# Optimization experiments

Hardware: AMD Instinct MI355X
Metric: run time of the kernel (lower is better)

The kernel has to match this reference:

```python
import jax, jax.numpy as jnp
import numpy as np
from jax import lax

PATCH = 3
RBF_SIGMA = 0.06 * PATCH ** 2      # module scales sigma by patch_size**2
SIG2 = RBF_SIGMA ** 2


def _unfold(img):
    # torch.nn.Unfold(kernel_size=3, stride=1): (b, c*9, N) with N=(H-2)*(W-2).
    # Channel ordering inside d differs from torch but distances sum over d,
    # so any consistent patch flattening yields identical math.
    p = lax.conv_general_dilated_patches(img, (PATCH, PATCH), (1, 1), 'VALID')
    b, d = p.shape[0], p.shape[1]
    return p.reshape(b, d, -1)  # (b, d, N)


def _kernel_mean(xu, yu):
    # mean over (N, M) of exp(-||x_i - y_j||^2 / sigma^2), via the
    # ||x||^2 + ||y||^2 - 2<x,y> expansion (avoids the (b,d,N,M) diff tensor).
    sqx = jnp.sum(xu * xu, axis=1)                   # (b, N)
    sqy = jnp.sum(yu * yu, axis=1)                   # (b, M)
    gram = jnp.einsum('bdn,bdm->bnm', xu, yu)        # (b, N, M)
    d2 = sqx[:, :, None] + sqy[:, None, :] - 2.0 * gram
    return jnp.mean(jnp.exp(-d2 / SIG2), axis=(1, 2))  # (b,)


def setup_inputs() -> dict:
    key = jax.random.key(0)
    kx, ky = jax.random.split(key)
    x = jax.random.normal(kx, (8, 3, 64, 64), dtype=jnp.float32)
    y = jax.random.normal(ky, (8, 3, 64, 64), dtype=jnp.float32)
    return {"x": x, "y": y}


def reference(x, y):
    xu = _unfold(x)
    yu = _unfold(y)
    batch_loss = (-2.0 * _kernel_mean(xu, yu)
                  + _kernel_mean(xu, xu)
                  + _kernel_mean(yu, yu))       # (b,)
    return jnp.mean(batch_loss)                 # batch_reduction='mean'
```

## Files before the change

### kernel.cpp

```cpp
#include <hip/hip_runtime.h>
#include <hip/hip_bf16.h>


#define NP    3844
#define NPAD  3968
#define KP    32

#define W_XY  7688
#define W_ALL 15624
#define NBLK  15624

static constexpr float L_F   = 4.9475824173972215f;
static constexpr float C2L_F = 9.895164834794443f;

using bf16x8 = __attribute__((ext_vector_type(8))) short;
using f32x4  = __attribute__((ext_vector_type(4))) float;

#define MFMA16(a, b, c) __builtin_amdgcn_mfma_f32_16x16x32_bf16((a), (b), (c), 0, 0, 0)

__device__ inline unsigned short f2bf(float f) {
    union { float f; unsigned u; } v; v.f = f;
    unsigned r = v.u + 0x7FFFu + ((v.u >> 16) & 1u);
    return (unsigned short)(r >> 16);
}
__device__ inline float bf2f(unsigned short h) {
    union { unsigned u; float f; } v; v.u = ((unsigned)h) << 16;
    return v.f;
}
__device__ inline void pack_store(unsigned short* dst, const unsigned short* v) {
    uint4* d = (uint4*)dst;
#pragma unroll
    for (int q = 0; q < 4; ++q) {
        unsigned w0 = (unsigned)v[8 * q + 0] | ((unsigned)v[8 * q + 1] << 16);
        unsigned w1 = (unsigned)v[8 * q + 2] | ((unsigned)v[8 * q + 3] << 16);
        unsigned w2 = (unsigned)v[8 * q + 4] | ((unsigned)v[8 * q + 5] << 16);
        unsigned w3 = (unsigned)v[8 * q + 6] | ((unsigned)v[8 * q + 7] << 16);
        d[q] = make_uint4(w0, w1, w2, w3);
    }
}

__global__ __launch_bounds__(256) void gp_prep(const float* __restrict__ x,
                                               const float* __restrict__ y,
                                               unsigned short* __restrict__ Am,
                                               unsigned short* __restrict__ Bm) {
    int i = blockIdx.x * 256 + threadIdx.x;
    if (i >= 16 * NPAD) return;
    int n = i % NPAD, im = i / NPAD;
    int b = im & 7;
    const float* src = (im >> 3) ? y : x;

    const unsigned short ONE = f2bf(1.0f);
    unsigned short hA[32], hB[32];
#pragma unroll
    for (int k = 0; k < 32; ++k) { hA[k] = 0; hB[k] = 0; }

    if (n < NP) {
        int r = n / 62, c = n % 62;
        float s = 0.0f;
#pragma unroll
        for (int ch = 0; ch < 3; ++ch)
#pragma unroll
            for (int pr = 0; pr < 3; ++pr)
#pragma unroll
                for (int pc = 0; pc < 3; ++pc) {
                    int k = ch * 9 + pr * 3 + pc;
                    float v = src[(((b * 3 + ch) * 64) + r + pr) * 64 + (c + pc)];
                    unsigned short ah = f2bf(C2L_F * v);
                    unsigned short bh = f2bf(v);
                    hA[k] = ah; hB[k] = bh;
                    s = fmaf(bf2f(ah), bf2f(bh), s);
                }
        float p = -0.5f * s;
        hA[27] = f2bf(p); hA[28] = f2bf(p - bf2f(hA[27]));
        hA[29] = ONE; hA[30] = ONE;
        hB[27] = ONE; hB[28] = ONE;
        hB[29] = f2bf(p); hB[30] = f2bf(p - bf2f(hB[29]));
    } else {
        hA[27] = f2bf(-1e30f); hA[29] = ONE; hA[30] = ONE;
        hB[27] = ONE; hB[28] = ONE; hB[29] = f2bf(-1e30f);
    }

    pack_store(Am + (size_t)i * KP, hA);
    pack_store(Bm + (size_t)i * KP, hB);
}

template<int OFF>
__device__ inline bf16x8 gload(const unsigned short* p) {
    bf16x8 r;
    asm volatile("global_load_dwordx4 %0, %1, off offset:%2"
                 : "=v"(r) : "v"(p), "i"(OFF));
    return r;
}

#define BODY(BHC)                                                            \
    do {                                                                     \
        const f32x4 Z = {0.f, 0.f, 0.f, 0.f};                                \
        f32x4 g0 = MFMA16(ah0, BHC, Z); f32x4 g1 = MFMA16(ah1, BHC, Z);      \
        f32x4 g2 = MFMA16(ah2, BHC, Z); f32x4 g3 = MFMA16(ah3, BHC, Z);      \
        f32x4 g4 = MFMA16(ah4, BHC, Z); f32x4 g5 = MFMA16(ah5, BHC, Z);      \
        f32x4 g6 = MFMA16(ah6, BHC, Z); f32x4 g7 = MFMA16(ah7, BHC, Z);      \
        float m0 = fmaxf(fmaxf(fmaxf(g0[0], g0[1]), g0[2]), g0[3]);          \
        float m1 = fmaxf(fmaxf(fmaxf(g1[0], g1[1]), g1[2]), g1[3]);          \
        float m2 = fmaxf(fmaxf(fmaxf(g2[0], g2[1]), g2[2]), g2[3]);          \
        float m3 = fmaxf(fmaxf(fmaxf(g3[0], g3[1]), g3[2]), g3[3]);          \
        float m4 = fmaxf(fmaxf(fmaxf(g4[0], g4[1]), g4[2]), g4[3]);          \
        float m5 = fmaxf(fmaxf(fmaxf(g5[0], g5[1]), g5[2]), g5[3]);          \
        float m6 = fmaxf(fmaxf(fmaxf(g6[0], g6[1]), g6[2]), g6[3]);          \
        float m7 = fmaxf(fmaxf(fmaxf(g7[0], g7[1]), g7[2]), g7[3]);          \
        float mm = fmaxf(fmaxf(fmaxf(fmaxf(fmaxf(fmaxf(fmaxf(m0, m1), m2),   \
                         m3), m4), m5), m6), m7);                            \
        if (__any(mm > -40.0f)) {                                            \
            s0 += __builtin_amdgcn_exp2f(g0[0]); s1 += __builtin_amdgcn_exp2f(g0[1]); \
            s2 += __builtin_amdgcn_exp2f(g0[2]); s3 += __builtin_amdgcn_exp2f(g0[3]); \
            s0 += __builtin_amdgcn_exp2f(g1[0]); s1 += __builtin_amdgcn_exp2f(g1[1]); \
            s2 += __builtin_amdgcn_exp2f(g1[2]); s3 += __builtin_amdgcn_exp2f(g1[3]); \
            s0 += __builtin_amdgcn_exp2f(g2[0]); s1 += __builtin_amdgcn_exp2f(g2[1]); \
            s2 += __builtin_amdgcn_exp2f(g2[2]); s3 += __builtin_amdgcn_exp2f(g2[3]); \
            s0 += __builtin_amdgcn_exp2f(g3[0]); s1 += __builtin_amdgcn_exp2f(g3[1]); \
            s2 += __builtin_amdgcn_exp2f(g3[2]); s3 += __builtin_amdgcn_exp2f(g3[3]); \
            s0 += __builtin_amdgcn_exp2f(g4[0]); s1 += __builtin_amdgcn_exp2f(g4[1]); \
            s2 += __builtin_amdgcn_exp2f(g4[2]); s3 += __builtin_amdgcn_exp2f(g4[3]); \
            s0 += __builtin_amdgcn_exp2f(g5[0]); s1 += __builtin_amdgcn_exp2f(g5[1]); \
            s2 += __builtin_amdgcn_exp2f(g5[2]); s3 += __builtin_amdgcn_exp2f(g5[3]); \
            s0 += __builtin_amdgcn_exp2f(g6[0]); s1 += __builtin_amdgcn_exp2f(g6[1]); \
            s2 += __builtin_amdgcn_exp2f(g6[2]); s3 += __builtin_amdgcn_exp2f(g6[3]); \
            s0 += __builtin_amdgcn_exp2f(g7[0]); s1 += __builtin_amdgcn_exp2f(g7[1]); \
            s2 += __builtin_amdgcn_exp2f(g7[2]); s3 += __builtin_amdgcn_exp2f(g7[3]); \
        }                                                                    \
    } while (0)

#define STEPN(N, CURREG)                                                     \
    do {                                                                     \
        asm volatile("s_waitcnt vmcnt(" #N ")" : "+v"(CURREG));              \
        __builtin_amdgcn_sched_barrier(0);                                   \
        BODY(CURREG);                                                        \
    } while (0)

__global__ __launch_bounds__(64, 4) void gp_pairs18(const unsigned short* __restrict__ Am,
                                                    const unsigned short* __restrict__ Bm,
                                                    float* __restrict__ part) {
    const int phys = blockIdx.x;
    const int w = (phys & 7) * 1953 + (phys >> 3);

    const int l = threadIdx.x & 63;
    const int l15 = l & 15, lhi = l >> 4;

    int type, b, bx, by, slot;
    float wt = 1.0f;
    if (w < W_XY) {
        type = 0; b = w / 961;
        int rr = w % 961; by = rr / 31; bx = rr % 31;
        slot = rr;
    } else {
        int v = w - W_XY;
        type = 1 + v / 3968;
        int r = v % 3968; b = r / 496; int t2 = r % 496;
        by = (int)((sqrtf(8.0f * (float)t2 + 1.0f) - 1.0f) * 0.5f);
        while ((by + 1) * (by + 2) / 2 <= t2) ++by;
        while (by * (by + 1) / 2 > t2) --by;
        bx = t2 - by * (by + 1) / 2;
        wt = (bx == by) ? 1.0f : 2.0f;
        slot = t2;
    }
    int imA, imB;
    if (type == 0)      { imA = b;     imB = 8 + b; }
    else if (type == 1) { imA = b;     imB = b;     }
    else                { imA = 8 + b; imB = 8 + b; }

    const size_t eA = ((size_t)(imA * NPAD + bx * 128 + l15)) * KP + lhi * 8;
    const size_t eB = ((size_t)(imB * NPAD + by * 128 + l15)) * KP + lhi * 8;
    const unsigned short* pA0 = Am + eA;
    const unsigned short* pA4 = pA0 + 2048;
    const unsigned short* pB0 = Bm + eB;
    const unsigned short* pB4 = pB0 + 2048;

    bf16x8 ah0 = gload<0>(pA0),    ah1 = gload<1024>(pA0);
    bf16x8 ah2 = gload<2048>(pA0), ah3 = gload<3072>(pA0);
    bf16x8 ah4 = gload<0>(pA4),    ah5 = gload<1024>(pA4);
    bf16x8 ah6 = gload<2048>(pA4), ah7 = gload<3072>(pA4);

    bf16x8 b0 = gload<0>(pB0),    b1 = gload<1024>(pB0);
    bf16x8 b2 = gload<2048>(pB0), b3 = gload<3072>(pB0);
    bf16x8 b4 = gload<0>(pB4),    b5 = gload<1024>(pB4);
    bf16x8 b6 = gload<2048>(pB4), b7 = gload<3072>(pB4);

    asm volatile("s_waitcnt vmcnt(8)"
                 : "+v"(ah0), "+v"(ah1), "+v"(ah2), "+v"(ah3),
                   "+v"(ah4), "+v"(ah5), "+v"(ah6), "+v"(ah7));
    __builtin_amdgcn_sched_barrier(0);

    float s0 = 0.f, s1 = 0.f, s2 = 0.f, s3 = 0.f;

    STEPN(7, b0);
    STEPN(6, b1);
    STEPN(5, b2);
    STEPN(4, b3);
    STEPN(3, b4);
    STEPN(2, b5);
    STEPN(1, b6);
    STEPN(0, b7);

    float sacc = wt * ((s0 + s1) + (s2 + s3));

#pragma unroll
    for (int o = 32; o > 0; o >>= 1) sacc += __shfl_down(sacc, o, 64);
    if (l == 0) part[(type * 8 + b) * 1024 + slot] = sacc;
}

__global__ __launch_bounds__(256) void gp_reduce(const float* __restrict__ part,
                                                 float* __restrict__ acc) {
    const int bkt = blockIdx.x;
    const int cnt = (bkt < 8) ? 961 : 496;
    const float* p = part + bkt * 1024;
    float s = 0.0f;
    for (int i = threadIdx.x; i < cnt; i += 256) s += p[i];
#pragma unroll
    for (int o = 32; o > 0; o >>= 1) s += __shfl_down(s, o, 64);
    __shared__ float red[4];
    if ((threadIdx.x & 63) == 0) red[threadIdx.x >> 6] = s;
    __syncthreads();
    if (threadIdx.x == 0) acc[bkt] = (red[0] + red[1]) + (red[2] + red[3]);
}

__global__ void gp_final(const float* __restrict__ acc, float* __restrict__ out) {
    if (threadIdx.x == 0) {
        double s = 0.0;
        for (int b = 0; b < 8; ++b)
            s += -2.0 * (double)acc[b] + (double)acc[8 + b] + (double)acc[16 + b];
        out[0] = (float)(s / (8.0 * (double)NP * (double)NP));
    }
}

extern "C" void kernel_launch(void* const* d_in, const int* in_sizes, int n_in,
                              void* d_out, int out_size, void* d_ws, size_t ws_size,
                              hipStream_t stream) {
    const float* x = (const float*)d_in[0];
    const float* y = (const float*)d_in[1];
    const size_t MSZ = (size_t)16 * NPAD * KP;
    unsigned short* Am = (unsigned short*)d_ws;
    unsigned short* Bm = Am + MSZ;
    float* acc = (float*)(Bm + MSZ);
    float* part = acc + 32;

    gp_prep<<<(16 * NPAD) / 256, 256, 0, stream>>>(x, y, Am, Bm);
    gp_pairs18<<<NBLK, 64, 0, stream>>>(Am, Bm, part);
    gp_reduce<<<24, 256, 0, stream>>>(part, acc);
    gp_final<<<1, 1, 0, stream>>>(acc, (float*)d_out);
}
```

Before: 39.56 us.

## Fuse reduction into pair kernel via last-block atomic and pack four waves per block

The pair kernel now runs four 64-lane waves per 256-thread block (3906 blocks instead of 15624 single-wave blocks), with an adjusted XCD-aware block-to-work mapping. The separate reduce and final kernels are removed. Each block writes its partials, bumps an atomic counter that gp_prep resets, and the last block to finish performs the 24-bucket reduction and writes the output. This removes two kernel launches and their gaps, at the cost of a block-level barrier in every block and a serialized tail reduction in one block.

```diff
diff --git a/kernel.cpp b/kernel.cpp
--- a/kernel.cpp
+++ b/kernel.cpp
@@ -8,7 +8,7 @@
 
 #define W_XY  7688
 #define W_ALL 15624
-#define NBLK  15624
+#define NBLK  3906
 
 static constexpr float L_F   = 4.9475824173972215f;
 static constexpr float C2L_F = 9.895164834794443f;
@@ -42,7 +42,9 @@
 __global__ __launch_bounds__(256) void gp_prep(const float* __restrict__ x,
                                                const float* __restrict__ y,
                                                unsigned short* __restrict__ Am,
-                                               unsigned short* __restrict__ Bm) {
+                                               unsigned short* __restrict__ Bm,
+                                               unsigned int* __restrict__ ctl) {
+    if (blockIdx.x == 0 && threadIdx.x == 0) ctl[0] = 0u;
     int i = blockIdx.x * 256 + threadIdx.x;
     if (i >= 16 * NPAD) return;
     int n = i % NPAD, im = i / NPAD;
@@ -136,14 +138,24 @@
         BODY(CURREG);                                                        \
     } while (0)
 
-__global__ __launch_bounds__(64, 4) void gp_pairs18(const unsigned short* __restrict__ Am,
-                                                    const unsigned short* __restrict__ Bm,
-                                                    float* __restrict__ part) {
+__global__ __launch_bounds__(256, 4) void gp_pairs19(const unsigned short* __restrict__ Am,
+                                                     const unsigned short* __restrict__ Bm,
+                                                     float* __restrict__ part,
+                                                     unsigned int* __restrict__ ctl,
+                                                     float* __restrict__ out) {
+    __shared__ int   sIdx[4];
+    __shared__ float sVal[4];
+    __shared__ int   sLast;
+    __shared__ float bsum[24];
+
     const int phys = blockIdx.x;
-    const int w = (phys & 7) * 1953 + (phys >> 3);
-
-    const int l = threadIdx.x & 63;
+    const int xcd = phys & 7, oi = phys >> 3;
+    const int blk = (xcd < 2 ? xcd * 489 : 2 * 489 + (xcd - 2) * 488) + oi;
+
+    const int t = threadIdx.x;
+    const int wv = t >> 6, l = t & 63;
     const int l15 = l & 15, lhi = l >> 4;
+    const int w = blk * 4 + wv;
 
     int type, b, bx, by, slot;
     float wt = 1.0f;
@@ -204,30 +216,39 @@
 
 #pragma unroll
     for (int o = 32; o > 0; o >>= 1) sacc += __shfl_down(sacc, o, 64);
-    if (l == 0) part[(type * 8 + b) * 1024 + slot] = sacc;
-}
-
-__global__ __launch_bounds__(256) void gp_reduce(const float* __restrict__ part,
-                                                 float* __restrict__ acc) {
-    const int bkt = blockIdx.x;
-    const int cnt = (bkt < 8) ? 961 : 496;
-    const float* p = part + bkt * 1024;
-    float s = 0.0f;
-    for (int i = threadIdx.x; i < cnt; i += 256) s += p[i];
-#pragma unroll
-    for (int o = 32; o > 0; o >>= 1) s += __shfl_down(s, o, 64);
-    __shared__ float red[4];
-    if ((threadIdx.x & 63) == 0) red[threadIdx.x >> 6] = s;
+    if (l == 0) { sIdx[wv] = (type * 8 + b) * 1024 + slot; sVal[wv] = sacc; }
     __syncthreads();
-    if (threadIdx.x == 0) acc[bkt] = (red[0] + red[1]) + (red[2] + red[3]);
-}
-
-__global__ void gp_final(const float* __restrict__ acc, float* __restrict__ out) {
-    if (threadIdx.x == 0) {
-        double s = 0.0;
-        for (int b = 0; b < 8; ++b)
-            s += -2.0 * (double)acc[b] + (double)acc[8 + b] + (double)acc[16 + b];
-        out[0] = (float)(s / (8.0 * (double)NP * (double)NP));
+
+    if (t == 0) {
+        part[sIdx[0]] = sVal[0];
+        part[sIdx[1]] = sVal[1];
+        part[sIdx[2]] = sVal[2];
+        part[sIdx[3]] = sVal[3];
+        __threadfence();
+        unsigned old = atomicAdd(ctl, 1u);
+        sLast = (old == (unsigned)(NBLK - 1)) ? 1 : 0;
+    }
+    __syncthreads();
+
+    if (sLast) {
+        __threadfence();
+        for (int bkt = wv; bkt < 24; bkt += 4) {
+            const int cnt = (bkt < 8) ? 961 : 496;
+            const float* p = part + bkt * 1024;
+            float s = 0.0f;
+            for (int i = l; i < cnt; i += 64) s += p[i];
+#pragma unroll
+            for (int o = 32; o > 0; o >>= 1) s += __shfl_down(s, o, 64);
+            if (l == 0) bsum[bkt] = s;
+        }
+        __syncthreads();
+        if (t == 0) {
+            double s = 0.0;
+            for (int b2 = 0; b2 < 8; ++b2)
+                s += -2.0 * (double)bsum[b2] + (double)bsum[8 + b2]
+                     + (double)bsum[16 + b2];
+            out[0] = (float)(s / (8.0 * (double)NP * (double)NP));
+        }
     }
 }
 
@@ -239,11 +260,9 @@
     const size_t MSZ = (size_t)16 * NPAD * KP;
     unsigned short* Am = (unsigned short*)d_ws;
     unsigned short* Bm = Am + MSZ;
-    float* acc = (float*)(Bm + MSZ);
-    float* part = acc + 32;
-
-    gp_prep<<<(16 * NPAD) / 256, 256, 0, stream>>>(x, y, Am, Bm);
-    gp_pairs18<<<NBLK, 64, 0, stream>>>(Am, Bm, part);
-    gp_reduce<<<24, 256, 0, stream>>>(part, acc);
-    gp_final<<<1, 1, 0, stream>>>(acc, (float*)d_out);
-}
+    unsigned int* ctl = (unsigned int*)(Bm + MSZ);
+    float* part = (float*)ctl + 32;
+
+    gp_prep<<<(16 * NPAD) / 256, 256, 0, stream>>>(x, y, Am, Bm, ctl);
+    gp_pairs19<<<NBLK, 256, 0, stream>>>(Am, Bm, part, ctl, (float*)d_out);
+}
```

Result: slower. 127.0 us (+221.1%).
